# Optimization experiments

Hardware: AMD Instinct MI355X
Metric: run time of the kernel (lower is better)

Reference implementation:

```python
import jax, jax.numpy as jnp
import numpy as np

H, CH, PQ, PV = 12, 16, 4, 8
C_S = 384
INF, EPS = 1e5, 1e-8
PT_W = -0.5


def setup_inputs() -> dict:
    key = jax.random.key(0)
    ks = jax.random.split(key, 20)
    B, C, N = 1, 8, 256
    s = jax.random.normal(ks[0], (B, C, N, C_S), jnp.float32)
    z = jax.random.normal(ks[1], (B, C, N, N, 8), jnp.float32)
    A = jax.random.normal(ks[2], (B, C, N, 3, 3), jnp.float32)
    rot = jnp.linalg.qr(A)[0]  # proper orthonormal frames
    trans = jax.random.normal(ks[3], (B, C, N, 3), jnp.float32) * 10.0
    mask = jnp.ones((B, C, N), jnp.float32)
    w = lambda k, i, o: jax.random.normal(k, (i, o), jnp.float32) * 0.02
    hc = H * CH
    return {
        's': s, 'z': z, 'rot': rot, 'trans': trans, 'mask': mask,
        'wq': w(ks[4], C_S, hc), 'bq': jnp.zeros((hc,)),
        'wkv': w(ks[5], C_S, 2 * hc), 'bkv': jnp.zeros((2 * hc,)),
        'g_gamma': jnp.ones((C_S,)), 'g_beta': jnp.zeros((C_S,)),
        'wgq': w(ks[6], C_S, hc), 'bgq': jnp.zeros((hc,)),
        'wgk': w(ks[7], C_S, hc), 'bgk': jnp.zeros((hc,)),
        'wqp': w(ks[8], C_S, H * PQ * 3), 'bqp': jnp.zeros((H * PQ * 3,)),
        'wkvp': w(ks[9], C_S, H * (PQ + PV) * 3), 'bkvp': jnp.zeros((H * (PQ + PV) * 3,)),
        'head_weights': jnp.full((H,), 0.5413248538970947, jnp.float32),  # softplus^-1(1)
        'wdist': w(ks[10], 1, H), 'bdist': jnp.zeros((H,)),
        'wout': w(ks[11], H * (CH + 4 * PV), C_S), 'bout': jnp.zeros((C_S,)),
    }


def _forward(s, z, rot, trans, mask, wq, bq, wkv, bkv, g_gamma, g_beta,
             wgq, bgq, wgk, bgk, wqp, bqp, wkvp, bkvp, head_weights,
             wdist, bdist, wout, bout):
    B, C, N, _ = s.shape
    q = (s @ wq + bq).reshape(B, C, N, H, CH)
    kv = (s @ wkv + bkv).reshape(B, C, N, H, 2 * CH)
    k, v = kv[..., :CH], kv[..., CH:]
    scale = (1.0 / (3 * CH)) ** 0.5
    a = jnp.einsum('bcihd,bcjhd->bchij', q, k) * scale  # [B,C,H,N,N]
    # global feature: mean over conformations, LayerNorm, QK bias
    s_g = s.mean(axis=-3)
    mu = s_g.mean(-1, keepdims=True)
    var = ((s_g - mu) ** 2).mean(-1, keepdims=True)
    s_gn = (s_g - mu) / jnp.sqrt(var + 1e-5) * g_gamma + g_beta
    g_q = (s_gn @ wgq + bgq).reshape(B, N, H, CH)
    g_k = (s_gn @ wgk + bgk).reshape(B, N, H, CH)
    a = a + jnp.einsum('bihd,bjhd->bhij', g_q, g_k)[:, None] * scale
    # invariant point attention term
    def to_pts(raw, P):
        pts = jnp.stack(jnp.split(raw, 3, axis=-1), axis=-1)  # [B,C,N,H*P,3]
        pts = jnp.einsum('bcnij,bcnpj->bcnpi', rot, pts) + trans[..., None, :]
        return pts.reshape(B, C, N, H, P, 3)
    q_pts = to_pts(s @ wqp + bqp, PQ)
    kv_pts = to_pts(s @ wkvp + bkvp, PQ + PV)
    k_pts, v_pts = kv_pts[..., :PQ, :], kv_pts[..., PQ:, :]
    diff2 = jnp.sum((q_pts[:, :, :, None] - k_pts[:, :, None]) ** 2, axis=-1)  # [B,C,N,N,H,PQ]
    hw = jax.nn.softplus(head_weights) * (1.0 / (3 * (PQ * 9.0 / 2))) ** 0.5
    pt_att = jnp.sum(diff2 * hw[:, None], axis=-1) * PT_W  # [B,C,N,N,H]
    a = a + jnp.moveaxis(pt_att, -1, -3)
    # mask
    sq_mask = mask[..., :, None] * mask[..., None, :]
    a = a + (INF * (sq_mask - 1.0))[..., None, :, :]
    # distance bias (torch uses a raw .view -> reshape, not transpose)
    dist = jnp.sqrt(jnp.sum((trans[..., :, None, :] - trans[..., None, :, :]) ** 2, axis=-1))
    db = dist[..., None] * wdist[0] + bdist  # [B,C,N,N,H]
    a = a + db.reshape(B, C, H, N, N)
    a = jax.nn.softmax(a, axis=-1)
    o = jnp.einsum('bchij,bcjhd->bcihd', a, v).reshape(B, C, N, H * CH)
    o_pt = jnp.einsum('bchij,bcjhpd->bcihpd', a, v_pts)  # [B,C,N,H,PV,3]
    o_pt = jnp.einsum('bcnji,bcnhpj->bcnhpi', rot, o_pt - trans[:, :, :, None, None, :])
    o_pt_norm = jnp.sqrt(jnp.sum(o_pt ** 2, axis=-1) + EPS).reshape(B, C, N, H * PV)
    o_pt_f = o_pt.reshape(B, C, N, H * PV, 3)
    feat = jnp.concatenate([o, o_pt_f[..., 0], o_pt_f[..., 1], o_pt_f[..., 2], o_pt_norm], axis=-1)
    return feat @ wout + bout, a


def reference(s, z, rot, trans, mask, wq, bq, wkv, bkv, g_gamma, g_beta,
              wgq, bgq, wgk, bgk, wqp, bqp, wkvp, bkvp, head_weights,
              wdist, bdist, wout, bout):
    return _forward(s, z, rot, trans, mask, wq, bq, wkv, bkv, g_gamma, g_beta,
                    wgq, bgq, wgk, bgk, wqp, bqp, wkvp, bkvp, head_weights,
                    wdist, bdist, wout, bout)
```

## Files before the change

### kernel.cpp

```cpp
#include <hip/hip_runtime.h>
#include <math.h>

#define NRES 256
#define CDIM 8
#define HNUM 12
#define CS   384

typedef __attribute__((ext_vector_type(8))) short bf16x8;
typedef __attribute__((ext_vector_type(4))) float f32x4;
typedef unsigned short ushort_t;

static __device__ __forceinline__ unsigned short f2bf(float x) {
    unsigned int u = __float_as_uint(x);
    unsigned int r = (u + 0x7fffu + ((u >> 16) & 1u)) >> 16;
    return (unsigned short)r;
}

__global__ __launch_bounds__(256) void convert_ln_kernel(
    const float* __restrict__ s,
    const float* __restrict__ wq, const float* __restrict__ bq,
    const float* __restrict__ wkv, const float* __restrict__ bkv,
    const float* __restrict__ wqp, const float* __restrict__ bqp,
    const float* __restrict__ wkvp, const float* __restrict__ bkvp,
    const float* __restrict__ wgq, const float* __restrict__ bgq,
    const float* __restrict__ wgk, const float* __restrict__ bgk,
    const float* __restrict__ wout,
    const float* __restrict__ g_gamma, const float* __restrict__ g_beta,
    ushort_t* __restrict__ s_bf, ushort_t* __restrict__ wt_bf,
    ushort_t* __restrict__ wtg_bf, float* __restrict__ pbias,
    float* __restrict__ gbias,
    ushort_t* __restrict__ wo_hi, ushort_t* __restrict__ wo_lo,
    ushort_t* __restrict__ sgn_bf)
{
    __shared__ float sg[CS];
    __shared__ float red[256];
    const int tid = threadIdx.x;
    const int NS   = 2048*384;
    const int NWT  = 384*1152;
    const int NWTG = 384*384;
    const int NWO  = 576*384;
    const int NB_CONV = 6246;

    if (blockIdx.x < NB_CONV) {
        const int idx = blockIdx.x*256 + tid;
        if (idx < NS) {
            s_bf[idx] = f2bf(s[idx]);
        } else if (idx < NS + NWT) {
            const int t = idx - NS;
            const int k = t / 1152, vc = t - k*1152;
            const float* w; int C, lc;
            if (vc < 192)      { w = wq;   C = 192; lc = vc; }
            else if (vc < 576) { w = wkv;  C = 384; lc = vc - 192; }
            else if (vc < 720) { w = wqp;  C = 144; lc = vc - 576; }
            else               { w = wkvp; C = 432; lc = vc - 720; }
            wt_bf[(size_t)vc*384 + k] = f2bf(w[(size_t)k*C + lc]);
        } else if (idx < NS + NWT + NWTG) {
            const int t = idx - NS - NWT;
            const int k = t / 384, vc = t - k*384;
            const float val = (vc < 192) ? wgq[(size_t)k*192 + vc]
                                         : wgk[(size_t)k*192 + vc - 192];
            wtg_bf[(size_t)vc*384 + k] = f2bf(val);
        } else if (idx < NS + NWT + NWTG + 1152) {
            const int i = idx - NS - NWT - NWTG;
            float b;
            if (i < 192)      b = bq[i];
            else if (i < 576) b = bkv[i - 192];
            else if (i < 720) b = bqp[i - 576];
            else              b = bkvp[i - 720];
            pbias[i] = b;
        } else if (idx < NS + NWT + NWTG + 1152 + 384) {
            const int i = idx - NS - NWT - NWTG - 1152;
            gbias[i] = (i < 192) ? bgq[i] : bgk[i - 192];
        } else if (idx < NS + NWT + NWTG + 1536 + NWO) {
            const int t = idx - NS - NWT - NWTG - 1536;
            const int k = t / 384, n = t - k*384;
            const float wv = wout[t];
            const unsigned int u = __float_as_uint(wv);
            const float hif = __uint_as_float(u & 0xFFFF0000u);
            wo_hi[(size_t)n*576 + k] = (ushort_t)(u >> 16);
            wo_lo[(size_t)n*576 + k] = (ushort_t)(__float_as_uint(wv - hif) >> 16);
        }
        return;
    }

    const int n = blockIdx.x - NB_CONV;
    for (int d = tid; d < CS; d += 256) {
        float acc = 0.f;
        for (int c = 0; c < CDIM; ++c) acc += s[((size_t)c*NRES+n)*CS + d];
        sg[d] = acc * (1.0f/CDIM);
    }
    __syncthreads();

    float lsum = 0.f;
    for (int d = tid; d < CS; d += 256) lsum += sg[d];
    red[tid] = lsum; __syncthreads();
    for (int st = 128; st > 0; st >>= 1) { if (tid < st) red[tid] += red[tid+st]; __syncthreads(); }
    const float mean = red[0] * (1.0f/CS);
    __syncthreads();

    float lvar = 0.f;
    for (int d = tid; d < CS; d += 256) { float df = sg[d]-mean; lvar += df*df; }
    red[tid] = lvar; __syncthreads();
    for (int st = 128; st > 0; st >>= 1) { if (tid < st) red[tid] += red[tid+st]; __syncthreads(); }
    const float var = red[0] * (1.0f/CS);
    __syncthreads();

    const float inv = rsqrtf(var + 1e-5f);
    for (int d = tid; d < CS; d += 256)
        sgn_bf[(size_t)n*CS + d] = f2bf((sg[d]-mean)*inv*g_gamma[d] + g_beta[d]);
}

__global__ __launch_bounds__(256) void proj_ggemm_kernel(
    const ushort_t* __restrict__ s_bf, const ushort_t* __restrict__ wt_bf,
    const float* __restrict__ pbias,
    const ushort_t* __restrict__ sgn_bf, const ushort_t* __restrict__ wtg_bf,
    const float* __restrict__ gbias,
    float* __restrict__ qo, float* __restrict__ ko, float* __restrict__ vo,
    float* __restrict__ rawp, float* __restrict__ gqo, float* __restrict__ gko)
{
    const int tid = threadIdx.x;
    const int wave = tid >> 6, lane = tid & 63;
    const int wrow = wave >> 1, wcol = wave & 1;
    const int qd = lane >> 4, lr = lane & 15;

    if (blockIdx.x < 576) {
        const int blk = blockIdx.x;
        const int rt = blk / 18, ct = blk - rt*18;
        const int r0 = rt * 64, c0 = ct * 64;
        const int m0 = r0 + wrow*32, n0 = c0 + wcol*32;

        f32x4 acc00 = {0,0,0,0}, acc01 = {0,0,0,0}, acc10 = {0,0,0,0}, acc11 = {0,0,0,0};

        const ushort_t* a0p = s_bf  + (size_t)(m0 + lr)*384 + qd*8;
        const ushort_t* a1p = a0p + 16*384;
        const ushort_t* b0p = wt_bf + (size_t)(n0 + lr)*384 + qd*8;
        const ushort_t* b1p = b0p + 16*384;

        #pragma unroll
        for (int kk = 0; kk < 384; kk += 32) {
            const bf16x8 a0 = *(const bf16x8*)(a0p + kk);
            const bf16x8 a1 = *(const bf16x8*)(a1p + kk);
            const bf16x8 b0 = *(const bf16x8*)(b0p + kk);
            const bf16x8 b1 = *(const bf16x8*)(b1p + kk);
            acc00 = __builtin_amdgcn_mfma_f32_16x16x32_bf16(a0, b0, acc00, 0, 0, 0);
            acc01 = __builtin_amdgcn_mfma_f32_16x16x32_bf16(a0, b1, acc01, 0, 0, 0);
            acc10 = __builtin_amdgcn_mfma_f32_16x16x32_bf16(a1, b0, acc10, 0, 0, 0);
            acc11 = __builtin_amdgcn_mfma_f32_16x16x32_bf16(a1, b1, acc11, 0, 0, 0);
        }

        #pragma unroll
        for (int mt = 0; mt < 2; ++mt) {
            #pragma unroll
            for (int nt = 0; nt < 2; ++nt) {
                const f32x4 av = (mt==0) ? (nt==0 ? acc00 : acc01)
                                         : (nt==0 ? acc10 : acc11);
                const int col = n0 + nt*16 + lr;
                const float bb = pbias[col];
                #pragma unroll
                for (int reg = 0; reg < 4; ++reg) {
                    const int row = m0 + mt*16 + qd*4 + reg;
                    const float val = av[reg] + bb;
                    if (col < 192) {
                        qo[(size_t)row*192 + col] = val;
                    } else if (col < 576) {
                        const int lc = col - 192, h = lc >> 5, rm = lc & 31;
                        if (rm < 16) ko[(size_t)row*192 + h*16 + rm] = val;
                        else         vo[(size_t)row*192 + h*16 + rm - 16] = val;
                    } else {
                        rawp[(size_t)row*576 + col - 576] = val;
                    }
                }
            }
        }
        return;
    }

    const int blk = blockIdx.x - 576;
    const int rt = blk / 6, ct = blk - rt*6;
    const int r0 = rt * 64, c0 = ct * 64;
    const int m0 = r0 + wrow*32, n0 = c0 + wcol*32;

    f32x4 acc00 = {0,0,0,0}, acc01 = {0,0,0,0}, acc10 = {0,0,0,0}, acc11 = {0,0,0,0};

    const ushort_t* a0p = sgn_bf + (size_t)(m0 + lr)*384 + qd*8;
    const ushort_t* a1p = a0p + 16*384;
    const ushort_t* b0p = wtg_bf + (size_t)(n0 + lr)*384 + qd*8;
    const ushort_t* b1p = b0p + 16*384;

    #pragma unroll
    for (int kk = 0; kk < 384; kk += 32) {
        const bf16x8 a0 = *(const bf16x8*)(a0p + kk);
        const bf16x8 a1 = *(const bf16x8*)(a1p + kk);
        const bf16x8 b0 = *(const bf16x8*)(b0p + kk);
        const bf16x8 b1 = *(const bf16x8*)(b1p + kk);
        acc00 = __builtin_amdgcn_mfma_f32_16x16x32_bf16(a0, b0, acc00, 0, 0, 0);
        acc01 = __builtin_amdgcn_mfma_f32_16x16x32_bf16(a0, b1, acc01, 0, 0, 0);
        acc10 = __builtin_amdgcn_mfma_f32_16x16x32_bf16(a1, b0, acc10, 0, 0, 0);
        acc11 = __builtin_amdgcn_mfma_f32_16x16x32_bf16(a1, b1, acc11, 0, 0, 0);
    }

    #pragma unroll
    for (int mt = 0; mt < 2; ++mt) {
        #pragma unroll
        for (int nt = 0; nt < 2; ++nt) {
            const f32x4 av = (mt==0) ? (nt==0 ? acc00 : acc01)
                                     : (nt==0 ? acc10 : acc11);
            const int col = n0 + nt*16 + lr;
            const float bb = gbias[col];
            #pragma unroll
            for (int reg = 0; reg < 4; ++reg) {
                const int row = m0 + mt*16 + qd*4 + reg;
                const float val = av[reg] + bb;
                if (col < 192) gqo[(size_t)row*192 + col]       = val;
                else           gko[(size_t)row*192 + col - 192] = val;
            }
        }
    }
}

#define BSTR 104
__global__ __launch_bounds__(256) void attn_mfma_kernel(
    const float* __restrict__ q, const float* __restrict__ k,
    const float* __restrict__ rawp, const float* __restrict__ rot,
    const float* __restrict__ g_q, const float* __restrict__ g_k,
    const float* __restrict__ trans, const float* __restrict__ mask,
    const float* __restrict__ head_weights, const float* __restrict__ wdist,
    const float* __restrict__ bdist, float* __restrict__ a_out)
{
    const int blk  = blockIdx.x;
    const int qtr  = blk & 3;
    const int ch   = blk >> 2;
    const int h    = ch % HNUM;
    const int c    = ch / HNUM;
    const int i0   = qtr * 64;
    const int tid  = threadIdx.x;

    __shared__ ushort_t Bsh[256*BSTR];
    __shared__ ushort_t Ash[64*BSTR];
    __shared__ float dsh[7*256];
    __shared__ float msh[256];
    __shared__ float kn_sh[256];
    __shared__ float qn_sh[64];
    __shared__ float wdsh[12], bdsh[12];
    __shared__ float cpart[96];
    __shared__ float censh[3];

    msh[tid] = mask[c*NRES + tid];
    if (tid < 12) { wdsh[tid] = wdist[tid]; bdsh[tid] = bdist[tid]; }

    if (tid < 96) {
        const int coord = tid % 3, chunk = tid / 3;
        float sv = 0.f;
        for (int e = 0; e < 8; ++e)
            sv += trans[((size_t)c*NRES + chunk*8 + e)*3 + coord];
        cpart[tid] = sv;
    }
    __syncthreads();
    if (tid < 3) {
        float sv = 0.f;
        for (int e = 0; e < 32; ++e) sv += cpart[e*3 + tid];
        censh[tid] = sv * (1.0f/256.0f);
    }
    __syncthreads();

    const float s54   = 0.13608276348795434f;
    const float scale = 0.14433756729740643f;
    const float hwv = 0.5f * logf(1.0f + expf(head_weights[h])) * s54;
    const float sh  = sqrtf(2.0f * hwv);
    const float cx = censh[0], cy = censh[1], cz = censh[2];

    {
        const int j = tid;
        const int grow = c*NRES + j;
        const float4* kr4 = (const float4*)(k   + (size_t)grow*192 + h*16);
        const float4* gk4 = (const float4*)(g_k + (size_t)j*192 + h*16);
        ushort_t* br = &Bsh[j*BSTR];
        #pragma unroll
        for (int e4 = 0; e4 < 4; ++e4) {
            const float4 w = kr4[e4];
            br[e4*4+0] = f2bf(w.x); br[e4*4+1] = f2bf(w.y);
            br[e4*4+2] = f2bf(w.z); br[e4*4+3] = f2bf(w.w);
        }
        #pragma unroll
        for (int e4 = 0; e4 < 4; ++e4) {
            const float4 w = gk4[e4];
            br[16+e4*4+0] = f2bf(w.x); br[16+e4*4+1] = f2bf(w.y);
            br[16+e4*4+2] = f2bf(w.z); br[16+e4*4+3] = f2bf(w.w);
        }
        const float* base = rawp + (size_t)grow*576;
        const float4 rx = *(const float4*)(base + 144 + h*12);
        const float4 ry = *(const float4*)(base + 288 + h*12);
        const float4 rz = *(const float4*)(base + 432 + h*12);
        const float* R = rot + (size_t)grow*9;
        const float* T = trans + (size_t)grow*3;
        const float R0=R[0],R1=R[1],R2=R[2],R3=R[3],R4=R[4],R5=R[5],R6=R[6],R7=R[7],R8=R[8];
        const float Tx=T[0]-cx, Ty=T[1]-cy, Tz=T[2]-cz;
        const float xs[4] = {rx.x, rx.y, rx.z, rx.w};
        const float ys[4] = {ry.x, ry.y, ry.z, ry.w};
        const float zs[4] = {rz.x, rz.y, rz.z, rz.w};
        float kn = 0.f;
        #pragma unroll
        for (int pp = 0; pp < 4; ++pp) {
            const float x = xs[pp], y = ys[pp], z = zs[pp];
            const float pv[3] = { R0*x + R1*y + R2*z + Tx,
                                  R3*x + R4*y + R5*z + Ty,
                                  R6*x + R7*y + R8*z + Tz };
            #pragma unroll
            for (int cc = 0; cc < 3; ++cc) {
                const int e = pp*3 + cc;
                kn += pv[cc]*pv[cc];
                const float sp = sh * pv[cc];
                const unsigned int u = __float_as_uint(sp);
                const float hif = __uint_as_float(u & 0xFFFF0000u);
                const ushort_t hi = (ushort_t)(u >> 16);
                br[32+e] = hi;
                br[44+e] = (ushort_t)(__float_as_uint(sp - hif) >> 16);
                br[56+e] = hi;
            }
        }
        #pragma unroll
        for (int e = 68; e < 96; ++e) br[e] = 0;
        kn_sh[j] = hwv * kn;
    }

    if (tid < 64) {
        const int il = i0 + tid;
        const int grow = c*NRES + il;
        const float4* qr4 = (const float4*)(q   + (size_t)grow*192 + h*16);
        const float4* gq4 = (const float4*)(g_q + (size_t)il*192 + h*16);
        ushort_t* ar = &Ash[tid*BSTR];
        #pragma unroll
        for (int e4 = 0; e4 < 4; ++e4) {
            const float4 w = qr4[e4];
            ar[e4*4+0] = f2bf(scale*w.x); ar[e4*4+1] = f2bf(scale*w.y);
            ar[e4*4+2] = f2bf(scale*w.z); ar[e4*4+3] = f2bf(scale*w.w);
        }
        #pragma unroll
        for (int e4 = 0; e4 < 4; ++e4) {
            const float4 w = gq4[e4];
            ar[16+e4*4+0] = f2bf(scale*w.x); ar[16+e4*4+1] = f2bf(scale*w.y);
            ar[16+e4*4+2] = f2bf(scale*w.z); ar[16+e4*4+3] = f2bf(scale*w.w);
        }
        const float* base = rawp + (size_t)grow*576;
        const float4 rx = *(const float4*)(base + h*4);
        const float4 ry = *(const float4*)(base + 48 + h*4);
        const float4 rz = *(const float4*)(base + 96 + h*4);
        const float* R = rot + (size_t)grow*9;
        const float* T = trans + (size_t)grow*3;
        const float R0=R[0],R1=R[1],R2=R[2],R3=R[3],R4=R[4],R5=R[5],R6=R[6],R7=R[7],R8=R[8];
        const float Tx=T[0]-cx, Ty=T[1]-cy, Tz=T[2]-cz;
        const float xs[4] = {rx.x, rx.y, rx.z, rx.w};
        const float ys[4] = {ry.x, ry.y, ry.z, ry.w};
        const float zs[4] = {rz.x, rz.y, rz.z, rz.w};
        float qn = 0.f;
        #pragma unroll
        for (int pp = 0; pp < 4; ++pp) {
            const float x = xs[pp], y = ys[pp], z = zs[pp];
            const float pv[3] = { R0*x + R1*y + R2*z + Tx,
                                  R3*x + R4*y + R5*z + Ty,
                                  R6*x + R7*y + R8*z + Tz };
            #pragma unroll
            for (int cc = 0; cc < 3; ++cc) {
                const int e = pp*3 + cc;
                qn += pv[cc]*pv[cc];
                const float sp = sh * pv[cc];
                const unsigned int u = __float_as_uint(sp);
                const float hif = __uint_as_float(u & 0xFFFF0000u);
                const ushort_t hi = (ushort_t)(u >> 16);
                ar[32+e] = hi;
                ar[44+e] = hi;
                ar[56+e] = (ushort_t)(__float_as_uint(sp - hif) >> 16);
            }
        }
        #pragma unroll
        for (int e = 68; e < 96; ++e) ar[e] = 0;
        qn_sh[tid] = hwv * qn;
    }

    const int Fmin = h*65536 + i0*256;
    const int iibase = Fmin / 3072;
    const int NI = (Fmin + 63*256 + 255)/3072 - iibase + 1;
    const float* tch = trans + (size_t)c*768;
    for (int idx = tid; idx < NI*256; idx += 256) {
        const int e = idx >> 8, jj = idx & 255;
        const int ia = iibase + e;
        const float dx = tch[ia*3+0] - tch[jj*3+0];
        const float dy = tch[ia*3+1] - tch[jj*3+1];
        const float dz = tch[ia*3+2] - tch[jj*3+2];
        dsh[idx] = sqrtf(dx*dx + dy*dy + dz*dz);
    }
    __syncthreads();

    const int wave = tid >> 6, lane = tid & 63;
    const int qd = lane >> 4, lr = lane & 15;
    const int m0 = wave*16;

    const ushort_t* ap = &Ash[(m0 + lr)*BSTR + qd*8];
    const bf16x8 af0 = *(const bf16x8*)(ap);
    const bf16x8 af1 = *(const bf16x8*)(ap + 32);
    const bf16x8 af2 = *(const bf16x8*)(ap + 64);

    f32x4 acc[16];
    #pragma unroll
    for (int t = 0; t < 16; ++t) {
        const ushort_t* bp = &Bsh[(t*16 + lr)*BSTR + qd*8];
        f32x4 a = {0.f,0.f,0.f,0.f};
        a = __builtin_amdgcn_mfma_f32_16x16x32_bf16(af0, *(const bf16x8*)(bp),      a, 0, 0, 0);
        a = __builtin_amdgcn_mfma_f32_16x16x32_bf16(af1, *(const bf16x8*)(bp + 32), a, 0, 0, 0);
        a = __builtin_amdgcn_mfma_f32_16x16x32_bf16(af2, *(const bf16x8*)(bp + 64), a, 0, 0, 0);
        acc[t] = a;
    }

    const int ibase = m0 + qd*4;
    float qn_r[4], mb_r[4];
    int F0_[4];
    #pragma unroll
    for (int r = 0; r < 4; ++r) {
        const int il = i0 + ibase + r;
        qn_r[r] = qn_sh[ibase + r];
        mb_r[r] = 100000.0f * msh[il];
        F0_[r]  = h*65536 + il*256;
    }

    float mx[4] = {-1e30f,-1e30f,-1e30f,-1e30f};
    #pragma unroll
    for (int t = 0; t < 16; ++t) {
        const int j = t*16 + lr;
        const float knj = kn_sh[j];
        const float mj  = msh[j];
        #pragma unroll
        for (int r = 0; r < 4; ++r) {
            const unsigned int f = (unsigned int)(F0_[r] + j);
            const unsigned int p = f / 12u;
            const int ho = (int)(f - p*12u);
            const int ii = (int)(p >> 8);
            const int jj = (int)(p & 255u);
            const float dist = dsh[(ii - iibase)*256 + jj];
            const float db = dist*wdsh[ho] + bdsh[ho];
            const float lv = acc[t][r] - qn_r[r] - knj
                           + (mb_r[r]*mj - 100000.0f) + db;
            acc[t][r] = lv;
            mx[r] = fmaxf(mx[r], lv);
        }
    }
    #pragma unroll
    for (int r = 0; r < 4; ++r) {
        #pragma unroll
        for (int off = 1; off < 16; off <<= 1)
            mx[r] = fmaxf(mx[r], __shfl_xor(mx[r], off));
    }
    float sm[4] = {0.f,0.f,0.f,0.f};
    #pragma unroll
    for (int t = 0; t < 16; ++t) {
        #pragma unroll
        for (int r = 0; r < 4; ++r) {
            const float e = __expf(acc[t][r] - mx[r]);
            acc[t][r] = e;
            sm[r] += e;
        }
    }
    #pragma unroll
    for (int r = 0; r < 4; ++r) {
        #pragma unroll
        for (int off = 1; off < 16; off <<= 1)
            sm[r] += __shfl_xor(sm[r], off);
        sm[r] = 1.0f / sm[r];
    }
    float* dst = a_out + ((size_t)ch*NRES + (i0 + ibase))*NRES;
    #pragma unroll
    for (int t = 0; t < 16; ++t) {
        #pragma unroll
        for (int r = 0; r < 4; ++r)
            dst[(size_t)r*NRES + t*16 + lr] = acc[t][r]*sm[r];
    }
}

#define ASTRB 264
__global__ __launch_bounds__(256) void out_feat_mfma_kernel(
    const float* __restrict__ a, const float* __restrict__ v,
    const float* __restrict__ rawp, const float* __restrict__ rot,
    const float* __restrict__ trans,
    ushort_t* __restrict__ feat_hi, ushort_t* __restrict__ feat_lo)
{
    const int blk = blockIdx.x;
    const int qtr = blk & 3;
    const int ch  = blk >> 2;
    const int h   = ch % HNUM;
    const int c   = ch / HNUM;
    const int i0  = qtr * 64;
    const int tid = threadIdx.x;

    __shared__ ushort_t Bt[64*ASTRB];
    __shared__ float opt[64*25];
    __shared__ float osh[64*17];
    __shared__ float cpart[96];
    __shared__ float censh[3];

    if (tid < 96) {
        const int coord = tid % 3, chunk = tid / 3;
        float sv = 0.f;
        for (int e = 0; e < 8; ++e)
            sv += trans[((size_t)c*NRES + chunk*8 + e)*3 + coord];
        cpart[tid] = sv;
    }
    __syncthreads();
    if (tid < 3) {
        float sv = 0.f;
        for (int e = 0; e < 32; ++e) sv += cpart[e*3 + tid];
        censh[tid] = sv * (1.0f/256.0f);
    }
    __syncthreads();
    const float cx = censh[0], cy = censh[1], cz = censh[2];

    {
        const int j = tid;
        const int grow = c*NRES + j;
        const float4* vr = (const float4*)(v + (size_t)grow*192 + h*16);
        #pragma unroll
        for (int e4 = 0; e4 < 4; ++e4) {
            const float4 w = vr[e4];
            Bt[(e4*4+0)*ASTRB + j] = f2bf(w.x);
            Bt[(e4*4+1)*ASTRB + j] = f2bf(w.y);
            Bt[(e4*4+2)*ASTRB + j] = f2bf(w.z);
            Bt[(e4*4+3)*ASTRB + j] = f2bf(w.w);
        }
        const float* base = rawp + (size_t)grow*576;
        const float4 rx0 = *(const float4*)(base + 144 + h*12 + 4);
        const float4 rx1 = *(const float4*)(base + 144 + h*12 + 8);
        const float4 ry0 = *(const float4*)(base + 288 + h*12 + 4);
        const float4 ry1 = *(const float4*)(base + 288 + h*12 + 8);
        const float4 rz0 = *(const float4*)(base + 432 + h*12 + 4);
        const float4 rz1 = *(const float4*)(base + 432 + h*12 + 8);
        const float* R = rot + (size_t)grow*9;
        const float* T = trans + (size_t)grow*3;
        const float R0=R[0],R1=R[1],R2=R[2],R3=R[3],R4=R[4],R5=R[5],R6=R[6],R7=R[7],R8=R[8];
        const float Tx=T[0]-cx, Ty=T[1]-cy, Tz=T[2]-cz;
        const float xs[8] = {rx0.x,rx0.y,rx0.z,rx0.w, rx1.x,rx1.y,rx1.z,rx1.w};
        const float ys[8] = {ry0.x,ry0.y,ry0.z,ry0.w, ry1.x,ry1.y,ry1.z,ry1.w};
        const float zs[8] = {rz0.x,rz0.y,rz0.z,rz0.w, rz1.x,rz1.y,rz1.z,rz1.w};
        #pragma unroll
        for (int pp = 0; pp < 8; ++pp) {
            const float x = xs[pp], y = ys[pp], z = zs[pp];
            const float pv[3] = { R0*x + R1*y + R2*z + Tx,
                                  R3*x + R4*y + R5*z + Ty,
                                  R6*x + R7*y + R8*z + Tz };
            #pragma unroll
            for (int cc = 0; cc < 3; ++cc) {
                const int e = pp*3 + cc;
                const float vp = pv[cc];
                const unsigned int u = __float_as_uint(vp);
                const float hif = __uint_as_float(u & 0xFFFF0000u);
                Bt[(16+e)*ASTRB + j] = (ushort_t)(u >> 16);
                Bt[(40+e)*ASTRB + j] = (ushort_t)(__float_as_uint(vp - hif) >> 16);
            }
        }
    }
    __syncthreads();

    const int wave = tid >> 6, lane = tid & 63;
    const int qd = lane >> 4, lr = lane & 15;
    const int m0 = wave*16;

    const float* arow = a + ((size_t)ch*NRES + i0 + m0 + lr)*NRES;

    f32x4 acc[4] = {{0,0,0,0},{0,0,0,0},{0,0,0,0},{0,0,0,0}};
    #pragma unroll
    for (int kk = 0; kk < 256; kk += 32) {
        const float4 a0 = *(const float4*)(arow + qd*8 + kk);
        const float4 a1 = *(const float4*)(arow + qd*8 + kk + 4);
        const float av[8] = {a0.x,a0.y,a0.z,a0.w,a1.x,a1.y,a1.z,a1.w};
        bf16x8 ahi, alo;
        #pragma unroll
        for (int e = 0; e < 8; ++e) {
            const unsigned int u = __float_as_uint(av[e]);
            const float hif = __uint_as_float(u & 0xFFFF0000u);
            ((ushort_t*)&ahi)[e] = (ushort_t)(u >> 16);
            ((ushort_t*)&alo)[e] = (ushort_t)(__float_as_uint(av[e] - hif) >> 16);
        }
        #pragma unroll
        for (int t = 0; t < 4; ++t) {
            const bf16x8 bf = *(const bf16x8*)&Bt[(t*16 + lr)*ASTRB + qd*8 + kk];
            acc[t] = __builtin_amdgcn_mfma_f32_16x16x32_bf16(ahi, bf, acc[t], 0, 0, 0);
            acc[t] = __builtin_amdgcn_mfma_f32_16x16x32_bf16(alo, bf, acc[t], 0, 0, 0);
        }
    }

    #pragma unroll
    for (int reg = 0; reg < 4; ++reg) {
        const int row_l = m0 + qd*4 + reg;
        osh[row_l*17 + lr] = acc[0][reg];
        opt[row_l*25 + lr] = acc[1][reg];
    }
    #pragma unroll
    for (int reg = 0; reg < 4; ++reg) {
        const int row_l = m0 + qd*4 + reg;
        if (lr < 8) opt[row_l*25 + 16 + lr] = acc[2][reg];
        else        opt[row_l*25 + (lr-8)] += acc[2][reg];
    }
    #pragma unroll
    for (int reg = 0; reg < 4; ++reg) {
        const int row_l = m0 + qd*4 + reg;
        opt[row_l*25 + 8 + lr] += acc[3][reg];
    }
    __syncthreads();

    #pragma unroll
    for (int it = 0; it < 4; ++it) {
        const int idx = it*256 + tid;
        const int row_l = idx >> 4, e = idx & 15;
        const int grow = c*NRES + i0 + row_l;
        const float val = osh[row_l*17 + e];
        const unsigned int u = __float_as_uint(val);
        const float hif = __uint_as_float(u & 0xFFFF0000u);
        feat_hi[(size_t)grow*576 + h*16 + e] = (ushort_t)(u >> 16);
        feat_lo[(size_t)grow*576 + h*16 + e] = (ushort_t)(__float_as_uint(val - hif) >> 16);
    }
    #pragma unroll
    for (int it = 0; it < 2; ++it) {
        const int idx = it*256 + tid;
        const int row_l = idx >> 3, p = idx & 7;
        const int grow = c*NRES + i0 + row_l;
        const float* R = rot + (size_t)grow*9;
        const float* T = trans + (size_t)grow*3;
        const float x = opt[row_l*25 + p*3+0] + cx - T[0];
        const float y = opt[row_l*25 + p*3+1] + cy - T[1];
        const float z = opt[row_l*25 + p*3+2] + cz - T[2];
        const float rx = R[0]*x + R[3]*y + R[6]*z;
        const float ry = R[1]*x + R[4]*y + R[7]*z;
        const float rz = R[2]*x + R[5]*y + R[8]*z;
        const float nm = sqrtf(rx*rx + ry*ry + rz*rz + 1e-8f);
        const float vals[4] = {rx, ry, rz, nm};
        #pragma unroll
        for (int sl = 0; sl < 4; ++sl) {
            const int col = 192 + sl*96 + h*8 + p;
            const float vv = vals[sl];
            const unsigned int u = __float_as_uint(vv);
            const float hif = __uint_as_float(u & 0xFFFF0000u);
            feat_hi[(size_t)grow*576 + col] = (ushort_t)(u >> 16);
            feat_lo[(size_t)grow*576 + col] = (ushort_t)(__float_as_uint(vv - hif) >> 16);
        }
    }
}

__global__ __launch_bounds__(256) void out_gemm_mfma_kernel(
    const ushort_t* __restrict__ feat_hi, const ushort_t* __restrict__ feat_lo,
    const ushort_t* __restrict__ wo_hi, const ushort_t* __restrict__ wo_lo,
    const float* __restrict__ bout, float* __restrict__ out0)
{
    const int blk = blockIdx.x;
    const int rt = blk / 6, ct = blk - rt*6;
    const int r0 = rt * 64, c0 = ct * 64;
    const int tid = threadIdx.x;
    const int wave = tid >> 6, lane = tid & 63;
    const int wrow = wave >> 1, wcol = wave & 1;
    const int m0 = r0 + wrow*32, n0 = c0 + wcol*32;
    const int qd = lane >> 4, lr = lane & 15;

    f32x4 acc[2][2] = {{{0,0,0,0},{0,0,0,0}},{{0,0,0,0},{0,0,0,0}}};

    const ushort_t* ah0 = feat_hi + (size_t)(m0 + lr)*576 + qd*8;
    const ushort_t* ah1 = ah0 + 16*576;
    const ushort_t* al0 = feat_lo + (size_t)(m0 + lr)*576 + qd*8;
    const ushort_t* al1 = al0 + 16*576;
    const ushort_t* bh0 = wo_hi + (size_t)(n0 + lr)*576 + qd*8;
    const ushort_t* bh1 = bh0 + 16*576;
    const ushort_t* bl0 = wo_lo + (size_t)(n0 + lr)*576 + qd*8;
    const ushort_t* bl1 = bl0 + 16*576;

    for (int kk = 0; kk < 576; kk += 32) {
        const bf16x8 fh0 = *(const bf16x8*)(ah0 + kk);
        const bf16x8 fh1 = *(const bf16x8*)(ah1 + kk);
        const bf16x8 fl0 = *(const bf16x8*)(al0 + kk);
        const bf16x8 fl1 = *(const bf16x8*)(al1 + kk);
        const bf16x8 wh0 = *(const bf16x8*)(bh0 + kk);
        const bf16x8 wh1 = *(const bf16x8*)(bh1 + kk);
        const bf16x8 wl0 = *(const bf16x8*)(bl0 + kk);
        const bf16x8 wl1 = *(const bf16x8*)(bl1 + kk);
        acc[0][0] = __builtin_amdgcn_mfma_f32_16x16x32_bf16(fh0, wh0, acc[0][0], 0, 0, 0);
        acc[0][1] = __builtin_amdgcn_mfma_f32_16x16x32_bf16(fh0, wh1, acc[0][1], 0, 0, 0);
        acc[1][0] = __builtin_amdgcn_mfma_f32_16x16x32_bf16(fh1, wh0, acc[1][0], 0, 0, 0);
        acc[1][1] = __builtin_amdgcn_mfma_f32_16x16x32_bf16(fh1, wh1, acc[1][1], 0, 0, 0);
        acc[0][0] = __builtin_amdgcn_mfma_f32_16x16x32_bf16(fl0, wh0, acc[0][0], 0, 0, 0);
        acc[0][1] = __builtin_amdgcn_mfma_f32_16x16x32_bf16(fl0, wh1, acc[0][1], 0, 0, 0);
        acc[1][0] = __builtin_amdgcn_mfma_f32_16x16x32_bf16(fl1, wh0, acc[1][0], 0, 0, 0);
        acc[1][1] = __builtin_amdgcn_mfma_f32_16x16x32_bf16(fl1, wh1, acc[1][1], 0, 0, 0);
        acc[0][0] = __builtin_amdgcn_mfma_f32_16x16x32_bf16(fh0, wl0, acc[0][0], 0, 0, 0);
        acc[0][1] = __builtin_amdgcn_mfma_f32_16x16x32_bf16(fh0, wl1, acc[0][1], 0, 0, 0);
        acc[1][0] = __builtin_amdgcn_mfma_f32_16x16x32_bf16(fh1, wl0, acc[1][0], 0, 0, 0);
        acc[1][1] = __builtin_amdgcn_mfma_f32_16x16x32_bf16(fh1, wl1, acc[1][1], 0, 0, 0);
    }

    #pragma unroll
    for (int mt = 0; mt < 2; ++mt) {
        #pragma unroll
        for (int nt = 0; nt < 2; ++nt) {
            const int col = n0 + nt*16 + lr;
            const float bb = bout[col];
            #pragma unroll
            for (int reg = 0; reg < 4; ++reg) {
                const int row = m0 + mt*16 + qd*4 + reg;
                out0[(size_t)row*CS + col] = acc[mt][nt][reg] + bb;
            }
        }
    }
}

extern "C" void kernel_launch(void* const* d_in, const int* in_sizes, int n_in,
                              void* d_out, int out_size, void* d_ws, size_t ws_size,
                              hipStream_t stream)
{
    const float* s     = (const float*)d_in[0];
    const float* rot   = (const float*)d_in[2];
    const float* trans = (const float*)d_in[3];
    const float* mask  = (const float*)d_in[4];
    const float* wq    = (const float*)d_in[5];
    const float* bq    = (const float*)d_in[6];
    const float* wkv   = (const float*)d_in[7];
    const float* bkv   = (const float*)d_in[8];
    const float* g_gamma = (const float*)d_in[9];
    const float* g_beta  = (const float*)d_in[10];
    const float* wgq   = (const float*)d_in[11];
    const float* bgq   = (const float*)d_in[12];
    const float* wgk   = (const float*)d_in[13];
    const float* bgk   = (const float*)d_in[14];
    const float* wqp   = (const float*)d_in[15];
    const float* bqp   = (const float*)d_in[16];
    const float* wkvp  = (const float*)d_in[17];
    const float* bkvp  = (const float*)d_in[18];
    const float* head_weights = (const float*)d_in[19];
    const float* wdist = (const float*)d_in[20];
    const float* bdist = (const float*)d_in[21];
    const float* wout  = (const float*)d_in[22];
    const float* bout  = (const float*)d_in[23];

    float* ws      = (float*)d_ws;
    float* q_buf   = ws + 0;
    float* gq_buf  = ws + 983040;
    float* gk_buf  = ws + 1032192;
    float* k_buf   = ws + 1081344;
    float* v_buf   = ws + 1474560;
    ushort_t* sgn_bf  = (ushort_t*)(ws + 1867776);
    ushort_t* feat_hi = (ushort_t*)(ws + 2457600);
    ushort_t* feat_lo = (ushort_t*)(ws + 3047424);
    ushort_t* wo_hi   = (ushort_t*)(ws + 3637248);
    ushort_t* wo_lo   = (ushort_t*)(ws + 3747840);
    float*    rawp    = ws + 4194304;

    float* out0  = (float*)d_out;
    float* a_out = out0 + 786432;
    ushort_t* s_bf   = (ushort_t*)(a_out);
    ushort_t* wt_bf  = (ushort_t*)(a_out + 393216);
    ushort_t* wtg_bf = (ushort_t*)(a_out + 614400);
    float*    pbias  = a_out + 688128;
    float*    gbias  = a_out + 689280;

    convert_ln_kernel<<<6502, 256, 0, stream>>>(s, wq, bq, wkv, bkv, wqp, bqp,
                                                wkvp, bkvp, wgq, bgq, wgk, bgk,
                                                wout, g_gamma, g_beta,
                                                s_bf, wt_bf, wtg_bf, pbias, gbias,
                                                wo_hi, wo_lo, sgn_bf);
    proj_ggemm_kernel<<<600, 256, 0, stream>>>(s_bf, wt_bf, pbias,
                                               sgn_bf, wtg_bf, gbias,
                                               q_buf, k_buf, v_buf, rawp,
                                               gq_buf, gk_buf);
    attn_mfma_kernel<<<384, 256, 0, stream>>>(q_buf, k_buf, rawp, rot,
                                              gq_buf, gk_buf, trans, mask,
                                              head_weights, wdist, bdist, a_out);
    out_feat_mfma_kernel<<<384, 256, 0, stream>>>(a_out, v_buf, rawp, rot, trans,
                                                  feat_hi, feat_lo);
    out_gemm_mfma_kernel<<<192, 256, 0, stream>>>(feat_hi, feat_lo, wo_hi, wo_lo,
                                                  bout, out0);
}
```

Before: 200.4 us.

## Tile weight transposes through shared memory, vectorize s conversion and row stores

The conversion kernel now converts s with float4 loads and packed 8-byte stores. The weight transposes (projection, global QK and output weights) go through 64x64 shared-memory tiles so both global reads and writes are coalesced, which cuts the grid from 6502 to 1223 blocks. In the attention kernel, each thread builds its bf16 A/B row in registers and writes it to LDS as 16-byte vectors instead of scalar ushort stores. The cost is extra LDS usage in the conversion kernel, more register pressure from the 96-element row arrays, and a risk of misaligned vector stores if BSTR is not a multiple of 8.

```diff
diff --git a/kernel.cpp b/kernel.cpp
--- a/kernel.cpp
+++ b/kernel.cpp
@@ -16,6 +16,8 @@
     return (unsigned short)r;
 }
 
+#define TSTR 66
+#define FSTR 65
 __global__ __launch_bounds__(256) void convert_ln_kernel(
     const float* __restrict__ s,
     const float* __restrict__ wq, const float* __restrict__ bq,
@@ -32,58 +34,111 @@
     ushort_t* __restrict__ wo_hi, ushort_t* __restrict__ wo_lo,
     ushort_t* __restrict__ sgn_bf)
 {
+    __shared__ ushort_t tile[64*TSTR];
+    __shared__ float ftile[64*FSTR];
     __shared__ float sg[CS];
     __shared__ float red[256];
     const int tid = threadIdx.x;
-    const int NS   = 2048*384;
-    const int NWT  = 384*1152;
-    const int NWTG = 384*384;
-    const int NWO  = 576*384;
-    const int NB_CONV = 6246;
-
-    if (blockIdx.x < NB_CONV) {
-        const int idx = blockIdx.x*256 + tid;
-        if (idx < NS) {
-            s_bf[idx] = f2bf(s[idx]);
-        } else if (idx < NS + NWT) {
-            const int t = idx - NS;
-            const int k = t / 1152, vc = t - k*1152;
+    const int b = blockIdx.x;
+
+    if (b < 768) {
+        const int idx = b*256 + tid;
+        const float4 v = ((const float4*)s)[idx];
+        unsigned int p0 = (unsigned int)f2bf(v.x) | ((unsigned int)f2bf(v.y) << 16);
+        unsigned int p1 = (unsigned int)f2bf(v.z) | ((unsigned int)f2bf(v.w) << 16);
+        uint2 pk; pk.x = p0; pk.y = p1;
+        *(uint2*)&s_bf[(size_t)idx*4] = pk;
+        return;
+    }
+    if (b < 876) {
+        const int t = b - 768;
+        const int vt = t / 6, kt = t - vt*6;
+        const int vc0 = vt*64, k0 = kt*64;
+        #pragma unroll
+        for (int it = 0; it < 16; ++it) {
+            const int kk = it*4 + (tid >> 6);
+            const int vv = tid & 63;
+            const int vc = vc0 + vv;
             const float* w; int C, lc;
             if (vc < 192)      { w = wq;   C = 192; lc = vc; }
             else if (vc < 576) { w = wkv;  C = 384; lc = vc - 192; }
             else if (vc < 720) { w = wqp;  C = 144; lc = vc - 576; }
             else               { w = wkvp; C = 432; lc = vc - 720; }
-            wt_bf[(size_t)vc*384 + k] = f2bf(w[(size_t)k*C + lc]);
-        } else if (idx < NS + NWT + NWTG) {
-            const int t = idx - NS - NWT;
-            const int k = t / 384, vc = t - k*384;
-            const float val = (vc < 192) ? wgq[(size_t)k*192 + vc]
-                                         : wgk[(size_t)k*192 + vc - 192];
-            wtg_bf[(size_t)vc*384 + k] = f2bf(val);
-        } else if (idx < NS + NWT + NWTG + 1152) {
-            const int i = idx - NS - NWT - NWTG;
-            float b;
-            if (i < 192)      b = bq[i];
-            else if (i < 576) b = bkv[i - 192];
-            else if (i < 720) b = bqp[i - 576];
-            else              b = bkvp[i - 720];
-            pbias[i] = b;
-        } else if (idx < NS + NWT + NWTG + 1152 + 384) {
-            const int i = idx - NS - NWT - NWTG - 1152;
-            gbias[i] = (i < 192) ? bgq[i] : bgk[i - 192];
-        } else if (idx < NS + NWT + NWTG + 1536 + NWO) {
-            const int t = idx - NS - NWT - NWTG - 1536;
-            const int k = t / 384, n = t - k*384;
-            const float wv = wout[t];
+            tile[vv*TSTR + kk] = f2bf(w[(size_t)(k0+kk)*C + lc]);
+        }
+        __syncthreads();
+        #pragma unroll
+        for (int it = 0; it < 16; ++it) {
+            const int vv = it*4 + (tid >> 6);
+            const int kk = tid & 63;
+            wt_bf[(size_t)(vc0+vv)*384 + k0 + kk] = tile[vv*TSTR + kk];
+        }
+        return;
+    }
+    if (b < 912) {
+        const int t = b - 876;
+        const int vt = t / 6, kt = t - vt*6;
+        const int vc0 = vt*64, k0 = kt*64;
+        #pragma unroll
+        for (int it = 0; it < 16; ++it) {
+            const int kk = it*4 + (tid >> 6);
+            const int vv = tid & 63;
+            const int vc = vc0 + vv;
+            const float val = (vc < 192) ? wgq[(size_t)(k0+kk)*192 + vc]
+                                         : wgk[(size_t)(k0+kk)*192 + vc - 192];
+            tile[vv*TSTR + kk] = f2bf(val);
+        }
+        __syncthreads();
+        #pragma unroll
+        for (int it = 0; it < 16; ++it) {
+            const int vv = it*4 + (tid >> 6);
+            const int kk = tid & 63;
+            wtg_bf[(size_t)(vc0+vv)*384 + k0 + kk] = tile[vv*TSTR + kk];
+        }
+        return;
+    }
+    if (b < 966) {
+        const int t = b - 912;
+        const int nt = t / 9, kt = t - nt*9;
+        const int n0 = nt*64, k0 = kt*64;
+        #pragma unroll
+        for (int it = 0; it < 16; ++it) {
+            const int kk = it*4 + (tid >> 6);
+            const int nn = tid & 63;
+            ftile[nn*FSTR + kk] = wout[(size_t)(k0+kk)*384 + n0 + nn];
+        }
+        __syncthreads();
+        #pragma unroll
+        for (int it = 0; it < 16; ++it) {
+            const int nn = it*4 + (tid >> 6);
+            const int kk = tid & 63;
+            const float wv = ftile[nn*FSTR + kk];
             const unsigned int u = __float_as_uint(wv);
             const float hif = __uint_as_float(u & 0xFFFF0000u);
-            wo_hi[(size_t)n*576 + k] = (ushort_t)(u >> 16);
-            wo_lo[(size_t)n*576 + k] = (ushort_t)(__float_as_uint(wv - hif) >> 16);
+            wo_hi[(size_t)(n0+nn)*576 + k0 + kk] = (ushort_t)(u >> 16);
+            wo_lo[(size_t)(n0+nn)*576 + k0 + kk] =
+                (ushort_t)(__float_as_uint(wv - hif) >> 16);
         }
         return;
     }
-
-    const int n = blockIdx.x - NB_CONV;
+    if (b == 966) {
+        for (int i = tid; i < 1536; i += 256) {
+            if (i < 1152) {
+                float bb;
+                if (i < 192)      bb = bq[i];
+                else if (i < 576) bb = bkv[i - 192];
+                else if (i < 720) bb = bqp[i - 576];
+                else              bb = bkvp[i - 720];
+                pbias[i] = bb;
+            } else {
+                const int g = i - 1152;
+                gbias[g] = (g < 192) ? bgq[g] : bgk[g - 192];
+            }
+        }
+        return;
+    }
+
+    const int n = b - 967;
     for (int d = tid; d < CS; d += 256) {
         float acc = 0.f;
         for (int c = 0; c < CDIM; ++c) acc += s[((size_t)c*NRES+n)*CS + d];
@@ -272,20 +327,20 @@
     {
         const int j = tid;
         const int grow = c*NRES + j;
+        ushort_t rowv[96];
         const float4* kr4 = (const float4*)(k   + (size_t)grow*192 + h*16);
         const float4* gk4 = (const float4*)(g_k + (size_t)j*192 + h*16);
-        ushort_t* br = &Bsh[j*BSTR];
         #pragma unroll
         for (int e4 = 0; e4 < 4; ++e4) {
             const float4 w = kr4[e4];
-            br[e4*4+0] = f2bf(w.x); br[e4*4+1] = f2bf(w.y);
-            br[e4*4+2] = f2bf(w.z); br[e4*4+3] = f2bf(w.w);
+            rowv[e4*4+0] = f2bf(w.x); rowv[e4*4+1] = f2bf(w.y);
+            rowv[e4*4+2] = f2bf(w.z); rowv[e4*4+3] = f2bf(w.w);
         }
         #pragma unroll
         for (int e4 = 0; e4 < 4; ++e4) {
             const float4 w = gk4[e4];
-            br[16+e4*4+0] = f2bf(w.x); br[16+e4*4+1] = f2bf(w.y);
-            br[16+e4*4+2] = f2bf(w.z); br[16+e4*4+3] = f2bf(w.w);
+            rowv[16+e4*4+0] = f2bf(w.x); rowv[16+e4*4+1] = f2bf(w.y);
+            rowv[16+e4*4+2] = f2bf(w.z); rowv[16+e4*4+3] = f2bf(w.w);
         }
         const float* base = rawp + (size_t)grow*576;
         const float4 rx = *(const float4*)(base + 144 + h*12);
@@ -313,33 +368,37 @@
                 const unsigned int u = __float_as_uint(sp);
                 const float hif = __uint_as_float(u & 0xFFFF0000u);
                 const ushort_t hi = (ushort_t)(u >> 16);
-                br[32+e] = hi;
-                br[44+e] = (ushort_t)(__float_as_uint(sp - hif) >> 16);
-                br[56+e] = hi;
+                rowv[32+e] = hi;
+                rowv[44+e] = (ushort_t)(__float_as_uint(sp - hif) >> 16);
+                rowv[56+e] = hi;
             }
         }
         #pragma unroll
-        for (int e = 68; e < 96; ++e) br[e] = 0;
+        for (int e = 68; e < 96; ++e) rowv[e] = 0;
+        ushort_t* br = &Bsh[j*BSTR];
+        #pragma unroll
+        for (int e8 = 0; e8 < 12; ++e8)
+            *(bf16x8*)(br + e8*8) = *(const bf16x8*)(rowv + e8*8);
         kn_sh[j] = hwv * kn;
     }
 
     if (tid < 64) {
         const int il = i0 + tid;
         const int grow = c*NRES + il;
+        ushort_t rowv[96];
         const float4* qr4 = (const float4*)(q   + (size_t)grow*192 + h*16);
         const float4* gq4 = (const float4*)(g_q + (size_t)il*192 + h*16);
-        ushort_t* ar = &Ash[tid*BSTR];
         #pragma unroll
         for (int e4 = 0; e4 < 4; ++e4) {
             const float4 w = qr4[e4];
-            ar[e4*4+0] = f2bf(scale*w.x); ar[e4*4+1] = f2bf(scale*w.y);
-            ar[e4*4+2] = f2bf(scale*w.z); ar[e4*4+3] = f2bf(scale*w.w);
+            rowv[e4*4+0] = f2bf(scale*w.x); rowv[e4*4+1] = f2bf(scale*w.y);
+            rowv[e4*4+2] = f2bf(scale*w.z); rowv[e4*4+3] = f2bf(scale*w.w);
         }
         #pragma unroll
         for (int e4 = 0; e4 < 4; ++e4) {
             const float4 w = gq4[e4];
-            ar[16+e4*4+0] = f2bf(scale*w.x); ar[16+e4*4+1] = f2bf(scale*w.y);
-            ar[16+e4*4+2] = f2bf(scale*w.z); ar[16+e4*4+3] = f2bf(scale*w.w);
+            rowv[16+e4*4+0] = f2bf(scale*w.x); rowv[16+e4*4+1] = f2bf(scale*w.y);
+            rowv[16+e4*4+2] = f2bf(scale*w.z); rowv[16+e4*4+3] = f2bf(scale*w.w);
         }
         const float* base = rawp + (size_t)grow*576;
         const float4 rx = *(const float4*)(base + h*4);
@@ -367,13 +426,17 @@
                 const unsigned int u = __float_as_uint(sp);
                 const float hif = __uint_as_float(u & 0xFFFF0000u);
                 const ushort_t hi = (ushort_t)(u >> 16);
-                ar[32+e] = hi;
-                ar[44+e] = hi;
-                ar[56+e] = (ushort_t)(__float_as_uint(sp - hif) >> 16);
+                rowv[32+e] = hi;
+                rowv[44+e] = hi;
+                rowv[56+e] = (ushort_t)(__float_as_uint(sp - hif) >> 16);
             }
         }
         #pragma unroll
-        for (int e = 68; e < 96; ++e) ar[e] = 0;
+        for (int e = 68; e < 96; ++e) rowv[e] = 0;
+        ushort_t* ar = &Ash[tid*BSTR];
+        #pragma unroll
+        for (int e8 = 0; e8 < 12; ++e8)
+            *(bf16x8*)(ar + e8*8) = *(const bf16x8*)(rowv + e8*8);
         qn_sh[tid] = hwv * qn;
     }
 
@@ -754,7 +817,7 @@
     float*    pbias  = a_out + 688128;
     float*    gbias  = a_out + 689280;
 
-    convert_ln_kernel<<<6502, 256, 0, stream>>>(s, wq, bq, wkv, bkv, wqp, bqp,
+    convert_ln_kernel<<<1223, 256, 0, stream>>>(s, wq, bq, wkv, bkv, wqp, bqp,
                                                 wkvp, bkvp, wgq, bgq, wgk, bgk,
                                                 wout, g_gamma, g_beta,
                                                 s_bf, wt_bf, wtg_bf, pbias, gbias,
```

Result: no change. 197.8 us, median of 2 (-1.3%).
